# Performance work log

Measured on AMD Instinct MI355X. Metric: run time of the kernel, lower is better.

## Reference

```python
import jax, jax.numpy as jnp
import numpy as np

HEADS = 16
EMBED = 1024
HEAD_DIM = EMBED // HEADS


def setup_inputs() -> dict:
    key = jax.random.key(0)
    ks = jax.random.split(key, 10)
    B, SQ, SKV = 2, 2048, 2048
    s = 1.0 / np.sqrt(HEAD_DIM)
    sd = 1.0 / np.sqrt(EMBED)
    return {
        "queries": jax.random.normal(ks[0], (B, SQ, EMBED), jnp.float32),
        "values": jax.random.normal(ks[1], (B, SKV, EMBED), jnp.float32),
        "heads": HEADS,
        "Wv": jax.random.normal(ks[2], (HEAD_DIM, HEAD_DIM), jnp.float32) * s,
        "bv": jax.random.normal(ks[3], (HEAD_DIM,), jnp.float32) * 0.02,
        "Wk": jax.random.normal(ks[4], (HEAD_DIM, HEAD_DIM), jnp.float32) * s,
        "bk": jax.random.normal(ks[5], (HEAD_DIM,), jnp.float32) * 0.02,
        "Wq": jax.random.normal(ks[6], (HEAD_DIM, HEAD_DIM), jnp.float32) * s,
        "bq": jax.random.normal(ks[7], (HEAD_DIM,), jnp.float32) * 0.02,
        "Wd": jax.random.normal(ks[8], (EMBED, EMBED), jnp.float32) * sd,
        "bd": jax.random.normal(ks[9], (EMBED,), jnp.float32) * 0.02,
    }


def reference(queries, values, heads, Wv, bv, Wk, bk, Wq, bq, Wd, bd):
    n, sq, e = queries.shape
    skv = values.shape[1]
    d = e // heads
    # reshape to per-head layout [b, s, h, d]
    q_in = queries.reshape(n, sq, heads, d)
    v_in = values.reshape(n, skv, heads, d)
    # shared per-head linear projections (torch Linear: x @ W.T + b)
    v = jnp.einsum("bshd,ed->bshe", v_in, Wv) + bv
    # quirk preserved: keys computed from the ALREADY-PROJECTED values
    k = jnp.einsum("bshd,ed->bshe", v, Wk) + bk
    q = jnp.einsum("bshd,ed->bshe", q_in, Wq) + bq
    # full O(n^2) score matrix [b, h, sq, skv] (as in source)
    scores = jnp.einsum("bqhd,bkhd->bhqk", q, k) / jnp.sqrt(jnp.asarray(d, q.dtype))
    attn = jax.nn.softmax(scores, axis=-1)
    out = jnp.einsum("bhqk,bkhd->bqhd", attn, v).reshape(n, sq, e)
    return out @ Wd.T + bd
```

## Files before the change

### kernel.cpp

```cpp
#include <hip/hip_runtime.h>
#include <hip/hip_bf16.h>
#include <hip/hip_fp16.h>
#include <math.h>

typedef _Float16 f16;
typedef _Float16 f16x8 __attribute__((ext_vector_type(8)));
typedef _Float16 f16x4 __attribute__((ext_vector_type(4)));
typedef _Float16 f16x2 __attribute__((ext_vector_type(2)));
typedef unsigned short u16x8v __attribute__((ext_vector_type(8)));
typedef float f32x4 __attribute__((ext_vector_type(4)));

namespace {
constexpr int B = 2;
constexpr int H = 16;
constexpr int S = 2048;
constexpr int D = 64;
constexpr int E = 1024;
constexpr float QSCALE = 0.125f * 1.4426950408889634f;
}

#define GLOBAL_LOAD_LDS16(gp, lp)                                              \
  __builtin_amdgcn_global_load_lds(                                            \
      (const __attribute__((address_space(1))) void*)(gp),                     \
      (__attribute__((address_space(3))) void*)(lp), 16, 0, 0)

__global__ __launch_bounds__(256) void prep(const float* __restrict__ Wd, f16* __restrict__ wd16,
                                            const float* __restrict__ Wk, const float* __restrict__ Wv,
                                            const float* __restrict__ bv, const float* __restrict__ bk,
                                            float* __restrict__ Wkv, float* __restrict__ bkv) {
  if (blockIdx.x < 1024) {
    const int i = blockIdx.x * 256 + threadIdx.x;
    const float4 f = ((const float4*)Wd)[i];
    f16x4 o;
    o.x = (f16)f.x; o.y = (f16)f.y; o.z = (f16)f.z; o.w = (f16)f.w;
    *(f16x4*)(wd16 + 4 * (size_t)i) = o;
  } else {
    const int g = (blockIdx.x - 1024) * 256 + threadIdx.x;
    const int i = g >> 6, j = g & 63;
    float s = 0.f;
#pragma unroll 16
    for (int d = 0; d < 64; ++d) s = fmaf(Wk[i * 64 + d], Wv[d * 64 + j], s);
    Wkv[g] = s;
    if (g < 64) {
      float bb = bk[g];
#pragma unroll 16
      for (int d = 0; d < 64; ++d) bb = fmaf(Wk[g * 64 + d], bv[d], bb);
      bkv[g] = bb;
    }
  }
}

__global__ __launch_bounds__(256) void proj3_mfma(const float* __restrict__ xq,
                                                  const float* __restrict__ xv,
                                                  const float* __restrict__ Wq,
                                                  const float* __restrict__ bq,
                                                  const float* __restrict__ Wv,
                                                  const float* __restrict__ bv,
                                                  const float* __restrict__ Wkv,
                                                  const float* __restrict__ bkv,
                                                  f16* __restrict__ qp,
                                                  f16* __restrict__ vp,
                                                  f16* __restrict__ kp) {
  const int which = blockIdx.y;
  const float* x = which ? xv : xq;

  const int t = threadIdx.x, lane = t & 63, w = t >> 6;
  const int l15 = lane & 15, quad = lane >> 4;
  const int m0 = (blockIdx.x * 4 + w) * 64;

  f16x8 af[4][2];
#pragma unroll
  for (int mt = 0; mt < 4; ++mt)
#pragma unroll
    for (int kc = 0; kc < 2; ++kc) {
      const float* g = x + (size_t)(m0 + mt * 16 + l15) * 64 + kc * 32 + quad * 8;
      const float4 a = *(const float4*)g, b2 = *(const float4*)(g + 4);
      f16x8 v;
      v[0]=(f16)a.x; v[1]=(f16)a.y; v[2]=(f16)a.z; v[3]=(f16)a.w;
      v[4]=(f16)b2.x; v[5]=(f16)b2.y; v[6]=(f16)b2.z; v[7]=(f16)b2.w;
      af[mt][kc] = v;
    }

  const int npass = which ? 2 : 1;
  for (int pass = 0; pass < npass; ++pass) {
    const float* W    = which ? (pass ? Wkv : Wv) : Wq;
    const float* bias = which ? (pass ? bkv : bv) : bq;
    f16* out          = which ? (pass ? kp : vp) : qp;
    const float scale = which ? 1.0f : QSCALE;

    f16x8 wf[4][2];
#pragma unroll
    for (int nt = 0; nt < 4; ++nt)
#pragma unroll
      for (int kc = 0; kc < 2; ++kc) {
        const float* g = W + (size_t)(nt * 16 + l15) * 64 + kc * 32 + quad * 8;
        const float4 a = *(const float4*)g, b2 = *(const float4*)(g + 4);
        f16x8 v;
        v[0]=(f16)a.x; v[1]=(f16)a.y; v[2]=(f16)a.z; v[3]=(f16)a.w;
        v[4]=(f16)b2.x; v[5]=(f16)b2.y; v[6]=(f16)b2.z; v[7]=(f16)b2.w;
        wf[nt][kc] = v;
      }

    f32x4 acc[4][4];
#pragma unroll
    for (int nt = 0; nt < 4; ++nt)
#pragma unroll
      for (int mt = 0; mt < 4; ++mt) acc[nt][mt] = (f32x4){0.f, 0.f, 0.f, 0.f};
#pragma unroll
    for (int kc = 0; kc < 2; ++kc)
#pragma unroll
      for (int nt = 0; nt < 4; ++nt)
#pragma unroll
        for (int mt = 0; mt < 4; ++mt)
          acc[nt][mt] = __builtin_amdgcn_mfma_f32_16x16x32_f16(wf[nt][kc], af[mt][kc], acc[nt][mt], 0, 0, 0);

    float4 bl4[4];
#pragma unroll
    for (int nt = 0; nt < 4; ++nt) bl4[nt] = *(const float4*)&bias[nt * 16 + quad * 4];

#pragma unroll
    for (int mt = 0; mt < 4; ++mt) {
      const int g = m0 + mt * 16 + l15;
      const int h = g & 15, bs_ = g >> 4;
      const int b = bs_ >> 11, s = bs_ & 2047;
      f16* o = out + ((size_t)(b * H + h) * S + s) * 64 + quad * 4;
#pragma unroll
      for (int nt = 0; nt < 4; ++nt) {
        const float p0 = (acc[nt][mt][0] + bl4[nt].x) * scale;
        const float p1 = (acc[nt][mt][1] + bl4[nt].y) * scale;
        const float p2 = (acc[nt][mt][2] + bl4[nt].z) * scale;
        const float p3 = (acc[nt][mt][3] + bl4[nt].w) * scale;
        union { f16x4 v4; f16x2 hh[2]; } u;
        u.hh[0] = __builtin_bit_cast(f16x2, __builtin_amdgcn_cvt_pkrtz(p0, p1));
        u.hh[1] = __builtin_bit_cast(f16x2, __builtin_amdgcn_cvt_pkrtz(p2, p3));
        *(f16x4*)(o + nt * 16) = u.v4;
      }
    }
  }
}

__global__ __launch_bounds__(256) void attn_mfma(const f16* __restrict__ qp,
                                                 const f16* __restrict__ kp,
                                                 const f16* __restrict__ vp,
                                                 f16* __restrict__ ao) {
  __shared__ f16 ks[2][64 * 64];
  __shared__ f16 vt[2][64 * 64];
  const int t = threadIdx.x, lane = t & 63, w = t >> 6;
  const int l15 = lane & 15, quad = lane >> 4;
  const int bh = blockIdx.x;
  const int q0 = blockIdx.y * 128;
  const f16* qbase = qp + ((size_t)bh * S + q0 + w * 32) * D;
  const f16* kbase = kp + (size_t)bh * S * D;
  const f16* vbase = vp + (size_t)bh * S * D;

  const int kr = t >> 2, kc2 = (t & 3) * 2;
  const int vd0 = (t >> 5) * 8;
  const int p0 = (t & 31) * 2;
  const int vkv = ((p0 >> 5) << 5) | (((p0 & 7) >> 2) << 4) | (((p0 >> 3) & 3) << 2) | (p0 & 3);
  const int vchunk = p0 >> 3, vsub = p0 & 7;

  f16x8 qf[2][2];
#pragma unroll
  for (int mt = 0; mt < 2; ++mt)
#pragma unroll
    for (int kc = 0; kc < 2; ++kc)
      qf[mt][kc] = *(const f16x8*)(qbase + (size_t)(mt * 16 + l15) * D + kc * 32 + quad * 8);

  f16x8 vb4;
#pragma unroll
  for (int j = 0; j < 8; ++j) vb4[j] = (l15 == 0) ? (f16)1.0f : (f16)0.0f;

  f32x4 O[2][5];
#pragma unroll
  for (int mt = 0; mt < 2; ++mt)
#pragma unroll
    for (int nt = 0; nt < 5; ++nt) O[mt][nt] = (f32x4){0.f, 0.f, 0.f, 0.f};

  u16x8v ka, kb2, va, vb2;
  {
    const f16* gk = kbase + (size_t)kr * D + kc2 * 8;
    ka  = *(const u16x8v*)gk;
    kb2 = *(const u16x8v*)(gk + 8);
    const f16* gv = vbase + (size_t)vkv * D + vd0;
    va  = *(const u16x8v*)gv;
    vb2 = *(const u16x8v*)(gv + D);
  }
  {
    *(u16x8v*)&ks[0][kr * 64 + ((kc2 ^ (kr & 7)) * 8)]       = ka;
    *(u16x8v*)&ks[0][kr * 64 + (((kc2 + 1) ^ (kr & 7)) * 8)] = kb2;
#pragma unroll
    for (int j = 0; j < 8; ++j) {
      const int d = vd0 + j;
      const unsigned pk = (unsigned)va[j] | ((unsigned)vb2[j] << 16);
      *(unsigned*)&vt[0][d * 64 + ((vchunk ^ (d & 7)) * 8) + vsub] = pk;
    }
  }

  int cur = 0;
  for (int kt = 0; kt < S / 64; ++kt) {
    if (kt + 1 < S / 64) {
      const f16* gk = kbase + ((size_t)(kt + 1) * 64 + kr) * D + kc2 * 8;
      ka  = *(const u16x8v*)gk;
      kb2 = *(const u16x8v*)(gk + 8);
      const f16* gv = vbase + ((size_t)(kt + 1) * 64 + vkv) * D + vd0;
      va  = *(const u16x8v*)gv;
      vb2 = *(const u16x8v*)(gv + D);
    }
    __asm__ volatile("s_waitcnt lgkmcnt(0)" ::: "memory");
    __builtin_amdgcn_s_barrier();
    __asm__ volatile("" ::: "memory");

    f32x4 sc[4][2];
#pragma unroll
    for (int nt = 0; nt < 4; ++nt)
#pragma unroll
      for (int mt = 0; mt < 2; ++mt) sc[nt][mt] = (f32x4){0.f, 0.f, 0.f, 0.f};
    __builtin_amdgcn_s_setprio(1);
#pragma unroll
    for (int kc = 0; kc < 2; ++kc)
#pragma unroll
      for (int nt = 0; nt < 4; ++nt) {
        const f16x8 kf = *(const f16x8*)&ks[cur][(nt * 16 + l15) * 64 + (((kc * 4 + quad) ^ (l15 & 7)) * 8)];
#pragma unroll
        for (int mt = 0; mt < 2; ++mt)
          sc[nt][mt] = __builtin_amdgcn_mfma_f32_16x16x32_f16(kf, qf[mt][kc], sc[nt][mt], 0, 0, 0);
      }
    __builtin_amdgcn_s_setprio(0);

    f16x8 pa[2][2];
#pragma unroll
    for (int mt = 0; mt < 2; ++mt)
#pragma unroll
      for (int kc = 0; kc < 2; ++kc) {
        const f32x4 s0 = sc[2 * kc][mt], s1 = sc[2 * kc + 1][mt];
        union { f16x8 v8; f16x2 h[4]; } u;
        u.h[0] = __builtin_bit_cast(f16x2, __builtin_amdgcn_cvt_pkrtz(
            __builtin_amdgcn_exp2f(s0[0]), __builtin_amdgcn_exp2f(s0[1])));
        u.h[1] = __builtin_bit_cast(f16x2, __builtin_amdgcn_cvt_pkrtz(
            __builtin_amdgcn_exp2f(s0[2]), __builtin_amdgcn_exp2f(s0[3])));
        u.h[2] = __builtin_bit_cast(f16x2, __builtin_amdgcn_cvt_pkrtz(
            __builtin_amdgcn_exp2f(s1[0]), __builtin_amdgcn_exp2f(s1[1])));
        u.h[3] = __builtin_bit_cast(f16x2, __builtin_amdgcn_cvt_pkrtz(
            __builtin_amdgcn_exp2f(s1[2]), __builtin_amdgcn_exp2f(s1[3])));
        pa[mt][kc] = u.v8;
      }

    __builtin_amdgcn_s_setprio(1);
#pragma unroll
    for (int kc = 0; kc < 2; ++kc) {
#pragma unroll
      for (int nt = 0; nt < 4; ++nt) {
        const f16x8 vbf = *(const f16x8*)&vt[cur][(nt * 16 + l15) * 64 + (((kc * 4 + quad) ^ (l15 & 7)) * 8)];
#pragma unroll
        for (int mt = 0; mt < 2; ++mt)
          O[mt][nt] = __builtin_amdgcn_mfma_f32_16x16x32_f16(pa[mt][kc], vbf, O[mt][nt], 0, 0, 0);
      }
#pragma unroll
      for (int mt = 0; mt < 2; ++mt)
        O[mt][4] = __builtin_amdgcn_mfma_f32_16x16x32_f16(pa[mt][kc], vb4, O[mt][4], 0, 0, 0);
    }
    __builtin_amdgcn_s_setprio(0);

    if (kt + 1 < S / 64) {
      const int nb = cur ^ 1;
      *(u16x8v*)&ks[nb][kr * 64 + ((kc2 ^ (kr & 7)) * 8)]       = ka;
      *(u16x8v*)&ks[nb][kr * 64 + (((kc2 + 1) ^ (kr & 7)) * 8)] = kb2;
#pragma unroll
      for (int j = 0; j < 8; ++j) {
        const int d = vd0 + j;
        const unsigned pk = (unsigned)va[j] | ((unsigned)vb2[j] << 16);
        *(unsigned*)&vt[nb][d * 64 + ((vchunk ^ (d & 7)) * 8) + vsub] = pk;
      }
    }
    cur ^= 1;
  }

  const int b = bh >> 4, h = bh & 15;
#pragma unroll
  for (int mt = 0; mt < 2; ++mt)
#pragma unroll
    for (int r = 0; r < 4; ++r) {
      const float l = __shfl(O[mt][4][r], quad << 4, 64);
      const float inv = 1.f / l;
      const int row = q0 + w * 32 + mt * 16 + quad * 4 + r;
      f16* o = ao + ((size_t)b * S + row) * E + h * D;
#pragma unroll
      for (int nt = 0; nt < 4; ++nt)
        o[nt * 16 + l15] = (f16)(O[mt][nt][r] * inv);
    }
}

__global__ __launch_bounds__(256) void dense_mfma(const f16* __restrict__ A,
                                                  const f16* __restrict__ Wd16,
                                                  const float* __restrict__ bd,
                                                  float* __restrict__ out) {
  __shared__ f16 as[2][128 * 64];
  __shared__ f16 bs[2][128 * 64];
  const int t = threadIdx.x;
  const int lane = t & 63;
  const int w = t >> 6;
  const int l15 = lane & 15;
  const int quad = lane >> 4;
  const int m0 = blockIdx.x * 128;
  const int n0 = blockIdx.y * 128;
  const int wm = (w >> 1) * 64, wn = (w & 1) * 64;

  const int srow = (lane >> 3);
  const int schunk = (lane & 7) ^ srow;
  const f16* ga0 = A    + (size_t)(m0 + w * 32 + srow) * E + schunk * 8;
  const f16* gb0 = Wd16 + (size_t)(n0 + w * 32 + srow) * E + schunk * 8;

  constexpr int NT = E / 64;

  f32x4 acc[4][4];
#pragma unroll
  for (int mt = 0; mt < 4; ++mt)
#pragma unroll
    for (int nt = 0; nt < 4; ++nt) acc[mt][nt] = (f32x4){0.f, 0.f, 0.f, 0.f};

#pragma unroll
  for (int i = 0; i < 4; ++i) {
    GLOBAL_LOAD_LDS16(ga0 + (size_t)(i * 8) * E, &as[0][(w * 32 + i * 8) * 64]);
    GLOBAL_LOAD_LDS16(gb0 + (size_t)(i * 8) * E, &bs[0][(w * 32 + i * 8) * 64]);
  }
  __syncthreads();

  int cur = 0;
  for (int kt = 0; kt < NT; ++kt) {
    if (kt + 1 < NT) {
      const int nb = cur ^ 1;
#pragma unroll
      for (int i = 0; i < 4; ++i) {
        GLOBAL_LOAD_LDS16(ga0 + (size_t)(i * 8) * E + (kt + 1) * 64, &as[nb][(w * 32 + i * 8) * 64]);
        GLOBAL_LOAD_LDS16(gb0 + (size_t)(i * 8) * E + (kt + 1) * 64, &bs[nb][(w * 32 + i * 8) * 64]);
      }
    }
    f16x8 af[4][2];
#pragma unroll
    for (int mt = 0; mt < 4; ++mt)
#pragma unroll
      for (int kc = 0; kc < 2; ++kc)
        af[mt][kc] = *(const f16x8*)&as[cur][(wm + mt * 16 + l15) * 64 + (((kc * 4 + quad) ^ (l15 & 7)) * 8)];
#pragma unroll
    for (int kc = 0; kc < 2; ++kc)
#pragma unroll
      for (int nt = 0; nt < 4; ++nt) {
        const f16x8 bf = *(const f16x8*)&bs[cur][(wn + nt * 16 + l15) * 64 + (((kc * 4 + quad) ^ (l15 & 7)) * 8)];
#pragma unroll
        for (int mt = 0; mt < 4; ++mt)
          acc[mt][nt] = __builtin_amdgcn_mfma_f32_16x16x32_f16(af[mt][kc], bf, acc[mt][nt], 0, 0, 0);
      }
    __syncthreads();
    cur ^= 1;
  }

#pragma unroll
  for (int nt = 0; nt < 4; ++nt) {
    const int col = n0 + wn + nt * 16 + l15;
    const float bdv = bd[col];
#pragma unroll
    for (int mt = 0; mt < 4; ++mt)
#pragma unroll
      for (int r = 0; r < 4; ++r)
        out[(size_t)(m0 + wm + mt * 16 + quad * 4 + r) * E + col] = acc[mt][nt][r] + bdv;
  }
}

extern "C" void kernel_launch(void* const* d_in, const int* in_sizes, int n_in,
                              void* d_out, int out_size, void* d_ws, size_t ws_size,
                              hipStream_t stream) {
  const float* queries = (const float*)d_in[0];
  const float* values  = (const float*)d_in[1];
  const float* Wv = (const float*)d_in[3];
  const float* bv = (const float*)d_in[4];
  const float* Wk = (const float*)d_in[5];
  const float* bk = (const float*)d_in[6];
  const float* Wq = (const float*)d_in[7];
  const float* bq = (const float*)d_in[8];
  const float* Wd = (const float*)d_in[9];
  const float* bd = (const float*)d_in[10];
  float* out = (float*)d_out;

  char* ws = (char*)d_ws;
  f16* qp    = (f16*)(ws);
  f16* kp    = (f16*)(ws + 8u * 1024 * 1024);
  f16* vp    = (f16*)(ws + 16u * 1024 * 1024);
  f16* ao    = (f16*)(ws + 24u * 1024 * 1024);
  f16* wd16  = (f16*)(ws + 32u * 1024 * 1024);
  float* wkv = (float*)(ws + 34u * 1024 * 1024);
  float* bkv = (float*)(ws + 34u * 1024 * 1024 + 16384);
  (void)ws_size; (void)in_sizes; (void)n_in; (void)out_size;

  prep<<<1040, 256, 0, stream>>>(Wd, wd16, Wk, Wv, bv, bk, wkv, bkv);
  proj3_mfma<<<dim3(256, 2), 256, 0, stream>>>(queries, values, Wq, bq, Wv, bv, wkv, bkv, qp, vp, kp);
  attn_mfma<<<dim3(B * H, S / 128), 256, 0, stream>>>(qp, kp, vp, ao);
  dense_mfma<<<dim3(B * S / 128, E / 128), 256, 0, stream>>>(ao, wd16, bd, out);
}
```

Measured before the change: 186.1 us.

## Load K fragments directly into registers in attention; shrink dense N-tile to 64

The attention kernel stops staging K through shared memory. Each wave now loads its K MFMA fragments straight from global memory into a double-buffered register array, and only V keeps the transposed LDS path, with the loop unrolled by two so the buffer indices are static. This removes the K LDS writes and reads but adds register pressure and redundant global loads, since all four waves fetch the same K tile. The dense GEMM tile is narrowed from 128x128 to 128x64, doubling the grid to give more blocks for occupancy, at the cost of more A-tile reloads.

```diff
diff --git a/kernel.cpp b/kernel.cpp
--- a/kernel.cpp
+++ b/kernel.cpp
@@ -143,7 +143,6 @@
                                                  const f16* __restrict__ kp,
                                                  const f16* __restrict__ vp,
                                                  f16* __restrict__ ao) {
-  __shared__ f16 ks[2][64 * 64];
   __shared__ f16 vt[2][64 * 64];
   const int t = threadIdx.x, lane = t & 63, w = t >> 6;
   const int l15 = lane & 15, quad = lane >> 4;
@@ -153,12 +152,13 @@
   const f16* kbase = kp + (size_t)bh * S * D;
   const f16* vbase = vp + (size_t)bh * S * D;
 
-  const int kr = t >> 2, kc2 = (t & 3) * 2;
   const int vd0 = (t >> 5) * 8;
   const int p0 = (t & 31) * 2;
   const int vkv = ((p0 >> 5) << 5) | (((p0 & 7) >> 2) << 4) | (((p0 >> 3) & 3) << 2) | (p0 & 3);
   const int vchunk = p0 >> 3, vsub = p0 & 7;
 
+  const f16* kfbase = kbase + (size_t)l15 * D + quad * 8;
+
   f16x8 qf[2][2];
 #pragma unroll
   for (int mt = 0; mt < 2; ++mt)
@@ -176,18 +176,18 @@
 #pragma unroll
     for (int nt = 0; nt < 5; ++nt) O[mt][nt] = (f32x4){0.f, 0.f, 0.f, 0.f};
 
-  u16x8v ka, kb2, va, vb2;
+  f16x8 kf[2][4][2];
+#pragma unroll
+  for (int nt = 0; nt < 4; ++nt)
+#pragma unroll
+    for (int kc = 0; kc < 2; ++kc)
+      kf[0][nt][kc] = *(const f16x8*)(kfbase + (size_t)(nt * 16) * D + kc * 32);
+
+  u16x8v va, vb2;
   {
-    const f16* gk = kbase + (size_t)kr * D + kc2 * 8;
-    ka  = *(const u16x8v*)gk;
-    kb2 = *(const u16x8v*)(gk + 8);
     const f16* gv = vbase + (size_t)vkv * D + vd0;
     va  = *(const u16x8v*)gv;
     vb2 = *(const u16x8v*)(gv + D);
-  }
-  {
-    *(u16x8v*)&ks[0][kr * 64 + ((kc2 ^ (kr & 7)) * 8)]       = ka;
-    *(u16x8v*)&ks[0][kr * 64 + (((kc2 + 1) ^ (kr & 7)) * 8)] = kb2;
 #pragma unroll
     for (int j = 0; j < 8; ++j) {
       const int d = vd0 + j;
@@ -196,83 +196,83 @@
     }
   }
 
-  int cur = 0;
-  for (int kt = 0; kt < S / 64; ++kt) {
-    if (kt + 1 < S / 64) {
-      const f16* gk = kbase + ((size_t)(kt + 1) * 64 + kr) * D + kc2 * 8;
-      ka  = *(const u16x8v*)gk;
-      kb2 = *(const u16x8v*)(gk + 8);
-      const f16* gv = vbase + ((size_t)(kt + 1) * 64 + vkv) * D + vd0;
-      va  = *(const u16x8v*)gv;
-      vb2 = *(const u16x8v*)(gv + D);
-    }
-    __asm__ volatile("s_waitcnt lgkmcnt(0)" ::: "memory");
-    __builtin_amdgcn_s_barrier();
-    __asm__ volatile("" ::: "memory");
-
-    f32x4 sc[4][2];
-#pragma unroll
-    for (int nt = 0; nt < 4; ++nt)
-#pragma unroll
-      for (int mt = 0; mt < 2; ++mt) sc[nt][mt] = (f32x4){0.f, 0.f, 0.f, 0.f};
-    __builtin_amdgcn_s_setprio(1);
-#pragma unroll
-    for (int kc = 0; kc < 2; ++kc)
-#pragma unroll
-      for (int nt = 0; nt < 4; ++nt) {
-        const f16x8 kf = *(const f16x8*)&ks[cur][(nt * 16 + l15) * 64 + (((kc * 4 + quad) ^ (l15 & 7)) * 8)];
+  for (int kt2 = 0; kt2 < S / 64; kt2 += 2) {
+#pragma unroll
+    for (int half = 0; half < 2; ++half) {
+      const int kt = kt2 + half;
+      if (kt + 1 < S / 64) {
+        const f16* kn = kfbase + (size_t)((kt + 1) * 64) * D;
+#pragma unroll
+        for (int nt = 0; nt < 4; ++nt)
+#pragma unroll
+          for (int kc = 0; kc < 2; ++kc)
+            kf[half ^ 1][nt][kc] = *(const f16x8*)(kn + (size_t)(nt * 16) * D + kc * 32);
+        const f16* gv = vbase + ((size_t)(kt + 1) * 64 + vkv) * D + vd0;
+        va  = *(const u16x8v*)gv;
+        vb2 = *(const u16x8v*)(gv + D);
+      }
+      __asm__ volatile("s_waitcnt lgkmcnt(0)" ::: "memory");
+      __builtin_amdgcn_s_barrier();
+      __asm__ volatile("" ::: "memory");
+
+      f32x4 sc[4][2];
+#pragma unroll
+      for (int nt = 0; nt < 4; ++nt)
+#pragma unroll
+        for (int mt = 0; mt < 2; ++mt) sc[nt][mt] = (f32x4){0.f, 0.f, 0.f, 0.f};
+      __builtin_amdgcn_s_setprio(1);
+#pragma unroll
+      for (int kc = 0; kc < 2; ++kc)
+#pragma unroll
+        for (int nt = 0; nt < 4; ++nt)
+#pragma unroll
+          for (int mt = 0; mt < 2; ++mt)
+            sc[nt][mt] = __builtin_amdgcn_mfma_f32_16x16x32_f16(kf[half][nt][kc], qf[mt][kc], sc[nt][mt], 0, 0, 0);
+      __builtin_amdgcn_s_setprio(0);
+
+      f16x8 pa[2][2];
+#pragma unroll
+      for (int mt = 0; mt < 2; ++mt)
+#pragma unroll
+        for (int kc = 0; kc < 2; ++kc) {
+          const f32x4 s0 = sc[2 * kc][mt], s1 = sc[2 * kc + 1][mt];
+          union { f16x8 v8; f16x2 h[4]; } u;
+          u.h[0] = __builtin_bit_cast(f16x2, __builtin_amdgcn_cvt_pkrtz(
+              __builtin_amdgcn_exp2f(s0[0]), __builtin_amdgcn_exp2f(s0[1])));
+          u.h[1] = __builtin_bit_cast(f16x2, __builtin_amdgcn_cvt_pkrtz(
+              __builtin_amdgcn_exp2f(s0[2]), __builtin_amdgcn_exp2f(s0[3])));
+          u.h[2] = __builtin_bit_cast(f16x2, __builtin_amdgcn_cvt_pkrtz(
+              __builtin_amdgcn_exp2f(s1[0]), __builtin_amdgcn_exp2f(s1[1])));
+          u.h[3] = __builtin_bit_cast(f16x2, __builtin_amdgcn_cvt_pkrtz(
+              __builtin_amdgcn_exp2f(s1[2]), __builtin_amdgcn_exp2f(s1[3])));
+          pa[mt][kc] = u.v8;
+        }
+
+      __builtin_amdgcn_s_setprio(1);
+#pragma unroll
+      for (int kc = 0; kc < 2; ++kc) {
+#pragma unroll
+        for (int nt = 0; nt < 4; ++nt) {
+          const f16x8 vbf = *(const f16x8*)&vt[half][(nt * 16 + l15) * 64 + (((kc * 4 + quad) ^ (l15 & 7)) * 8)];
+#pragma unroll
+          for (int mt = 0; mt < 2; ++mt)
+            O[mt][nt] = __builtin_amdgcn_mfma_f32_16x16x32_f16(pa[mt][kc], vbf, O[mt][nt], 0, 0, 0);
+        }
 #pragma unroll
         for (int mt = 0; mt < 2; ++mt)
-          sc[nt][mt] = __builtin_amdgcn_mfma_f32_16x16x32_f16(kf, qf[mt][kc], sc[nt][mt], 0, 0, 0);
-      }
-    __builtin_amdgcn_s_setprio(0);
-
-    f16x8 pa[2][2];
-#pragma unroll
-    for (int mt = 0; mt < 2; ++mt)
-#pragma unroll
-      for (int kc = 0; kc < 2; ++kc) {
-        const f32x4 s0 = sc[2 * kc][mt], s1 = sc[2 * kc + 1][mt];
-        union { f16x8 v8; f16x2 h[4]; } u;
-        u.h[0] = __builtin_bit_cast(f16x2, __builtin_amdgcn_cvt_pkrtz(
-            __builtin_amdgcn_exp2f(s0[0]), __builtin_amdgcn_exp2f(s0[1])));
-        u.h[1] = __builtin_bit_cast(f16x2, __builtin_amdgcn_cvt_pkrtz(
-            __builtin_amdgcn_exp2f(s0[2]), __builtin_amdgcn_exp2f(s0[3])));
-        u.h[2] = __builtin_bit_cast(f16x2, __builtin_amdgcn_cvt_pkrtz(
-            __builtin_amdgcn_exp2f(s1[0]), __builtin_amdgcn_exp2f(s1[1])));
-        u.h[3] = __builtin_bit_cast(f16x2, __builtin_amdgcn_cvt_pkrtz(
-            __builtin_amdgcn_exp2f(s1[2]), __builtin_amdgcn_exp2f(s1[3])));
-        pa[mt][kc] = u.v8;
-      }
-
-    __builtin_amdgcn_s_setprio(1);
-#pragma unroll
-    for (int kc = 0; kc < 2; ++kc) {
-#pragma unroll
-      for (int nt = 0; nt < 4; ++nt) {
-        const f16x8 vbf = *(const f16x8*)&vt[cur][(nt * 16 + l15) * 64 + (((kc * 4 + quad) ^ (l15 & 7)) * 8)];
-#pragma unroll
-        for (int mt = 0; mt < 2; ++mt)
-          O[mt][nt] = __builtin_amdgcn_mfma_f32_16x16x32_f16(pa[mt][kc], vbf, O[mt][nt], 0, 0, 0);
-      }
-#pragma unroll
-      for (int mt = 0; mt < 2; ++mt)
-        O[mt][4] = __builtin_amdgcn_mfma_f32_16x16x32_f16(pa[mt][kc], vb4, O[mt][4], 0, 0, 0);
-    }
-    __builtin_amdgcn_s_setprio(0);
-
-    if (kt + 1 < S / 64) {
-      const int nb = cur ^ 1;
-      *(u16x8v*)&ks[nb][kr * 64 + ((kc2 ^ (kr & 7)) * 8)]       = ka;
-      *(u16x8v*)&ks[nb][kr * 64 + (((kc2 + 1) ^ (kr & 7)) * 8)] = kb2;
-#pragma unroll
-      for (int j = 0; j < 8; ++j) {
-        const int d = vd0 + j;
-        const unsigned pk = (unsigned)va[j] | ((unsigned)vb2[j] << 16);
-        *(unsigned*)&vt[nb][d * 64 + ((vchunk ^ (d & 7)) * 8) + vsub] = pk;
-      }
-    }
-    cur ^= 1;
+          O[mt][4] = __builtin_amdgcn_mfma_f32_16x16x32_f16(pa[mt][kc], vb4, O[mt][4], 0, 0, 0);
+      }
+      __builtin_amdgcn_s_setprio(0);
+
+      if (kt + 1 < S / 64) {
+#pragma unroll
+        for (int j = 0; j < 8; ++j) {
+          const int d = vd0 + j;
+          const unsigned pk = (unsigned)va[j] | ((unsigned)vb2[j] << 16);
+          *(unsigned*)&vt[half ^ 1][d * 64 + ((vchunk ^ (d & 7)) * 8) + vsub] = pk;
+        }
+      }
+    }
   }
 
   const int b = bh >> 4, h = bh & 15;
@@ -295,34 +295,35 @@
                                                   const float* __restrict__ bd,
                                                   float* __restrict__ out) {
   __shared__ f16 as[2][128 * 64];
-  __shared__ f16 bs[2][128 * 64];
+  __shared__ f16 bs[2][64 * 64];
   const int t = threadIdx.x;
   const int lane = t & 63;
   const int w = t >> 6;
   const int l15 = lane & 15;
   const int quad = lane >> 4;
   const int m0 = blockIdx.x * 128;
-  const int n0 = blockIdx.y * 128;
-  const int wm = (w >> 1) * 64, wn = (w & 1) * 64;
+  const int n0 = blockIdx.y * 64;
+  const int wm = (w >> 1) * 64, wn = (w & 1) * 32;
 
   const int srow = (lane >> 3);
   const int schunk = (lane & 7) ^ srow;
   const f16* ga0 = A    + (size_t)(m0 + w * 32 + srow) * E + schunk * 8;
-  const f16* gb0 = Wd16 + (size_t)(n0 + w * 32 + srow) * E + schunk * 8;
+  const f16* gb0 = Wd16 + (size_t)(n0 + w * 16 + srow) * E + schunk * 8;
 
   constexpr int NT = E / 64;
 
-  f32x4 acc[4][4];
+  f32x4 acc[4][2];
 #pragma unroll
   for (int mt = 0; mt < 4; ++mt)
 #pragma unroll
-    for (int nt = 0; nt < 4; ++nt) acc[mt][nt] = (f32x4){0.f, 0.f, 0.f, 0.f};
-
-#pragma unroll
-  for (int i = 0; i < 4; ++i) {
+    for (int nt = 0; nt < 2; ++nt) acc[mt][nt] = (f32x4){0.f, 0.f, 0.f, 0.f};
+
+#pragma unroll
+  for (int i = 0; i < 4; ++i)
     GLOBAL_LOAD_LDS16(ga0 + (size_t)(i * 8) * E, &as[0][(w * 32 + i * 8) * 64]);
-    GLOBAL_LOAD_LDS16(gb0 + (size_t)(i * 8) * E, &bs[0][(w * 32 + i * 8) * 64]);
-  }
+#pragma unroll
+  for (int i = 0; i < 2; ++i)
+    GLOBAL_LOAD_LDS16(gb0 + (size_t)(i * 8) * E, &bs[0][(w * 16 + i * 8) * 64]);
   __syncthreads();
 
   int cur = 0;
@@ -330,10 +331,11 @@
     if (kt + 1 < NT) {
       const int nb = cur ^ 1;
 #pragma unroll
-      for (int i = 0; i < 4; ++i) {
+      for (int i = 0; i < 4; ++i)
         GLOBAL_LOAD_LDS16(ga0 + (size_t)(i * 8) * E + (kt + 1) * 64, &as[nb][(w * 32 + i * 8) * 64]);
-        GLOBAL_LOAD_LDS16(gb0 + (size_t)(i * 8) * E + (kt + 1) * 64, &bs[nb][(w * 32 + i * 8) * 64]);
-      }
+#pragma unroll
+      for (int i = 0; i < 2; ++i)
+        GLOBAL_LOAD_LDS16(gb0 + (size_t)(i * 8) * E + (kt + 1) * 64, &bs[nb][(w * 16 + i * 8) * 64]);
     }
     f16x8 af[4][2];
 #pragma unroll
@@ -344,7 +346,7 @@
 #pragma unroll
     for (int kc = 0; kc < 2; ++kc)
 #pragma unroll
-      for (int nt = 0; nt < 4; ++nt) {
+      for (int nt = 0; nt < 2; ++nt) {
         const f16x8 bf = *(const f16x8*)&bs[cur][(wn + nt * 16 + l15) * 64 + (((kc * 4 + quad) ^ (l15 & 7)) * 8)];
 #pragma unroll
         for (int mt = 0; mt < 4; ++mt)
@@ -355,7 +357,7 @@
   }
 
 #pragma unroll
-  for (int nt = 0; nt < 4; ++nt) {
+  for (int nt = 0; nt < 2; ++nt) {
     const int col = n0 + wn + nt * 16 + l15;
     const float bdv = bd[col];
 #pragma unroll
@@ -394,5 +396,5 @@
   prep<<<1040, 256, 0, stream>>>(Wd, wd16, Wk, Wv, bv, bk, wkv, bkv);
   proj3_mfma<<<dim3(256, 2), 256, 0, stream>>>(queries, values, Wq, bq, Wv, bv, wkv, bkv, qp, vp, kp);
   attn_mfma<<<dim3(B * H, S / 128), 256, 0, stream>>>(qp, kp, vp, ao);
-  dense_mfma<<<dim3(B * S / 128, E / 128), 256, 0, stream>>>(ao, wd16, bd, out);
-}
+  dense_mfma<<<dim3(B * S / 128, E / 64), 256, 0, stream>>>(ao, wd16, bd, out);
+}
```

Result: slower. 206.7 us (+11.1%).
